# Kernel tuning notes

Measured on AMD Instinct MI355X. Metric: run time of the kernel, lower is better.

The kernel has to match this reference:

```python
import jax, jax.numpy as jnp
import numpy as np

C = 128        # dim_in = dim_out = dim_mid (exp_ratio=1.0)
HEADS = 4      # C // dim_head
DH = 32        # dim_head
WS = 7         # window_size
EPS = 1e-6
SCALE = DH ** -0.5


def bn3d(x, g, b):
    # BatchNorm3d forward (training-mode batch stats), eps=1e-6
    m = jnp.mean(x, axis=(0, 2, 3, 4), keepdims=True)
    v = jnp.mean((x - m) ** 2, axis=(0, 2, 3, 4), keepdims=True)
    xn = (x - m) * jax.lax.rsqrt(v + EPS)
    return xn * g.reshape(1, -1, 1, 1, 1) + b.reshape(1, -1, 1, 1, 1)


def conv1x1(x, w):
    # 1x1x1 conv, no bias: w is (out, in)
    return jnp.einsum('oi,bihwd->bohwd', w, x)


def setup_inputs() -> dict:
    key = jax.random.key(0)
    ks = jax.random.split(key, 6)
    x = jax.random.normal(ks[0], (4, C, 28, 28, 28), jnp.float32)
    g_in = jnp.ones((C,), jnp.float32)
    b_in = jnp.zeros((C,), jnp.float32)
    w_qk = jax.random.normal(ks[1], (2 * C, C), jnp.float32) * (C ** -0.5)
    w_v = jax.random.normal(ks[2], (C, C), jnp.float32) * (C ** -0.5)
    w_cl = jax.random.normal(ks[3], (C, C, 3, 3, 3), jnp.float32) * ((C * 27) ** -0.5)
    g_cl = jnp.ones((C,), jnp.float32)
    b_cl = jnp.zeros((C,), jnp.float32)
    w_proj = jax.random.normal(ks[4], (C, C), jnp.float32) * (C ** -0.5)
    return {"x": x, "g_in": g_in, "b_in": b_in, "w_qk": w_qk, "w_v": w_v,
            "w_cl": w_cl, "g_cl": g_cl, "b_cl": b_cl, "w_proj": w_proj}


def reference(x, g_in, b_in, w_qk, w_v, w_cl, g_cl, b_cl, w_proj):
    B, Cc, H, W, D = x.shape
    shortcut = x
    x = bn3d(x, g_in, b_in)

    # strided window partition: einops '(h1 n1)' => h1 (window) is the OUTER factor
    n1, n2, n3 = H // WS, W // WS, D // WS  # chosen divisible -> zero pad
    xw = x.reshape(B, Cc, WS, n1, WS, n2, WS, n3)
    xw = xw.transpose(0, 3, 5, 7, 1, 2, 4, 6).reshape(B * n1 * n2 * n3, Cc, WS, WS, WS)
    b = xw.shape[0]
    L = WS ** 3

    # qk: 1x1 conv -> split q,k -> (b, heads, L, dh)
    qk = conv1x1(xw, w_qk).reshape(b, 2, HEADS, DH, L)
    q = qk[:, 0].transpose(0, 1, 3, 2)       # b h L d
    k = qk[:, 1]                             # b h d L
    attn = jax.nn.softmax(jnp.einsum('bhld,bhdm->bhlm', q, k) * SCALE, axis=-1)

    # v: 1x1 conv + relu (attn_pre=False)
    v = jax.nn.relu(conv1x1(xw, w_v)).reshape(b, HEADS, DH, L)  # b h d L
    xs = jnp.einsum('bhlm,bhdm->bhld', attn, v)                 # b h L d
    xs = xs.transpose(0, 1, 3, 2).reshape(b, Cc, WS, WS, WS)

    # reverse window partition
    x = xs.reshape(B, n1, n2, n3, Cc, WS, WS, WS)
    x = x.transpose(0, 4, 5, 1, 6, 2, 7, 3).reshape(B, Cc, H, W, D)

    # local 3x3x3 conv + BN + SiLU, residual (has_skip inside iRMB branch)
    y = jax.lax.conv_general_dilated(
        x, w_cl, window_strides=(1, 1, 1),
        padding=[(1, 1), (1, 1), (1, 1)],
        dimension_numbers=('NCDHW', 'OIDHW', 'NCDHW'))
    y = jax.nn.silu(bn3d(y, g_cl, b_cl))
    x = x + y  # SE is Identity (se_ratio=0)

    x = conv1x1(x, w_proj)
    return shortcut + x
```

## Files before the change

### kernel.cpp

```cpp
#include <hip/hip_runtime.h>
#include <hip/hip_bf16.h>

#define C      128
#define SP     21952
#define PT     87808
#define LW     343
#define EPS_   1e-6f
#define SCALE_ 0.17677669529663687f

#define MISC_A   0
#define MISC_B   128
#define MISC_BQK 256
#define MISC_BV  512
#define MISC_SUM 640
#define MISC_SQ  768
#define MISC_A2  896
#define MISC_B2  1024
#define MISC_XS  1152
#define MISC_XQ  1280

typedef __attribute__((ext_vector_type(8))) short bf16x8;
typedef __attribute__((ext_vector_type(4))) float f32x4;

__device__ __forceinline__ float b2f(unsigned short u){
  return __uint_as_float(((unsigned int)u) << 16);
}
__device__ __forceinline__ unsigned short f2b(float f){
  unsigned int u = __float_as_uint(f);
  u += 0x7fffu + ((u >> 16) & 1u);
  return (unsigned short)(u >> 16);
}

__global__ __launch_bounds__(256) void k0_partial(const float* __restrict__ x,
                                                  float* __restrict__ misc){
  int c = blockIdx.x & 127, chunk = blockIdx.x >> 7;
  int bb = chunk >> 1, half = chunk & 1;
  const float4* p = reinterpret_cast<const float4*>(
      x + (size_t)(bb*C + c)*SP + half*10976);
  int t = threadIdx.x;
  float s = 0.f, ss = 0.f;
  for (int i = t; i < 2744; i += 256){
    float4 v = p[i];
    s  += v.x + v.y + v.z + v.w;
    ss += v.x*v.x + v.y*v.y + v.z*v.z + v.w*v.w;
  }
  #pragma unroll
  for (int off = 32; off > 0; off >>= 1){
    s  += __shfl_xor(s,  off);
    ss += __shfl_xor(ss, off);
  }
  __shared__ float red[8];
  int wid = t >> 6, lane = t & 63;
  if (lane == 0){ red[wid] = s; red[4+wid] = ss; }
  __syncthreads();
  if (t == 0){
    atomicAdd(&misc[MISC_XS + c], red[0]+red[1]+red[2]+red[3]);
    atomicAdd(&misc[MISC_XQ + c], red[4]+red[5]+red[6]+red[7]);
  }
}

__global__ void k1_bias(const float* __restrict__ wqk, const float* __restrict__ wvv,
                        const float* __restrict__ gin, const float* __restrict__ bin,
                        float* __restrict__ misc){
  __shared__ float bv[128];
  int t = threadIdx.x;
  {
    float mean = misc[MISC_XS + t] / (float)PT;
    float var  = misc[MISC_XQ + t] / (float)PT - mean*mean;
    float a = rsqrtf(var + EPS_) * gin[t];
    float bb = bin[t] - mean * a;
    bv[t] = bb;
    if (blockIdx.x == 0){ misc[MISC_A + t] = a; misc[MISC_B + t] = bb; }
  }
  __syncthreads();
  int o = blockIdx.x*128 + t;
  float acc = 0.f;
  if (o < 256){
    const float* wr = wqk + (size_t)o*128;
    for (int c = 0; c < 128; ++c) acc += wr[c]*bv[c];
    misc[MISC_BQK + o] = acc;
  } else {
    const float* wr = wvv + (size_t)(o-256)*128;
    for (int c = 0; c < 128; ++c) acc += wr[c]*bv[c];
    misc[MISC_BV + (o-256)] = acc;
  }
}

__global__ void k1w(const float* __restrict__ wqk, const float* __restrict__ wvv,
                    unsigned short* __restrict__ w2){
  int idx = blockIdx.x*256 + threadIdx.x;
  int o = idx >> 7;
  float w = (o < 256) ? wqk[idx] : wvv[idx - 32768];
  unsigned short h = f2b(w);
  w2[idx] = h;
  w2[49152 + idx] = f2b(w - b2f(h));
}

__global__ __launch_bounds__(256) void k2_qkv(const float* __restrict__ x,
        const unsigned short* __restrict__ w2, const float* __restrict__ misc,
        unsigned short* __restrict__ qg, unsigned short* __restrict__ kg,
        unsigned short* __restrict__ vg){
  __shared__ __align__(16) unsigned short xh[8192];
  __shared__ __align__(16) unsigned short xl[8192];
  __shared__ float ascale[128];
  __shared__ unsigned int posTab[64];
  int t = threadIdx.x;
  int P0 = blockIdx.x * 64;
  int b = P0 / SP, sp0 = P0 % SP;
  if (t < 128) ascale[t] = misc[MISC_A + t];
  if (t < 64){
    int sp = sp0 + t;
    int h_ = sp / 784, rem = sp % 784;
    int w_ = rem / 28, d_ = rem % 28;
    int w1 = h_ & 3, s1 = h_ >> 2;
    int w2i = w_ & 3, s2 = w_ >> 2;
    int w3 = d_ & 3, s3 = d_ >> 2;
    int bw = ((b*4 + w1)*4 + w2i)*4 + w3;
    int l  = (s1*7 + s2)*7 + s3;
    posTab[t] = (unsigned int)(bw*43904 + l*32);
  }
  __syncthreads();
  {
    int p = t & 63;
    int ob = t >> 6;
    const float* xb = x + (size_t)b*C*SP + sp0 + p;
    for (int it = 0; it < 4; ++it){
      int c0 = (ob + it*4) * 8;
      unsigned int ph[4], pl[4];
      #pragma unroll
      for (int j = 0; j < 4; ++j){
        float f0 = xb[(size_t)(c0 + 2*j)*SP]     * ascale[c0 + 2*j];
        float f1 = xb[(size_t)(c0 + 2*j + 1)*SP] * ascale[c0 + 2*j + 1];
        unsigned short h0 = f2b(f0), h1 = f2b(f1);
        unsigned short l0 = f2b(f0 - b2f(h0)), l1 = f2b(f1 - b2f(h1));
        ph[j] = (unsigned int)h0 | ((unsigned int)h1 << 16);
        pl[j] = (unsigned int)l0 | ((unsigned int)l1 << 16);
      }
      int byte = (p*256 + c0*2) ^ ((p & 7) << 4);
      *reinterpret_cast<uint4*>((char*)xh + byte) = make_uint4(ph[0],ph[1],ph[2],ph[3]);
      *reinterpret_cast<uint4*>((char*)xl + byte) = make_uint4(pl[0],pl[1],pl[2],pl[3]);
    }
  }
  __syncthreads();
  int wid = t >> 6, lane = t & 63;
  int g = lane >> 4, ln = lane & 15;
  int wstart = wid * 96;
  f32x4 acc[6][4];
  #pragma unroll
  for (int nt = 0; nt < 6; ++nt){
    float bv = misc[256 + wstart + nt*16 + ln];
    #pragma unroll
    for (int mt = 0; mt < 4; ++mt) acc[nt][mt] = (f32x4){bv,bv,bv,bv};
  }
  #pragma unroll 1
  for (int kk = 0; kk < 4; ++kk){
    bf16x8 ah[4], al[4];
    #pragma unroll
    for (int mt = 0; mt < 4; ++mt){
      int row = mt*16 + ln;
      int byte = (row*256 + kk*64 + g*16) ^ ((ln & 7) << 4);
      ah[mt] = *reinterpret_cast<const bf16x8*>((const char*)xh + byte);
      al[mt] = *reinterpret_cast<const bf16x8*>((const char*)xl + byte);
    }
    #pragma unroll
    for (int nt = 0; nt < 6; ++nt){
      int o = wstart + nt*16 + ln;
      const unsigned short* wp = w2 + (size_t)o*128 + kk*32 + g*8;
      bf16x8 whf = *reinterpret_cast<const bf16x8*>(wp);
      bf16x8 wlf = *reinterpret_cast<const bf16x8*>(wp + 49152);
      #pragma unroll
      for (int mt = 0; mt < 4; ++mt){
        acc[nt][mt] = __builtin_amdgcn_mfma_f32_16x16x32_bf16(ah[mt], whf, acc[nt][mt], 0, 0, 0);
        acc[nt][mt] = __builtin_amdgcn_mfma_f32_16x16x32_bf16(al[mt], whf, acc[nt][mt], 0, 0, 0);
        acc[nt][mt] = __builtin_amdgcn_mfma_f32_16x16x32_bf16(ah[mt], wlf, acc[nt][mt], 0, 0, 0);
      }
    }
  }
  unsigned int ptab[16];
  #pragma unroll
  for (int mt = 0; mt < 4; ++mt)
    #pragma unroll
    for (int r = 0; r < 4; ++r)
      ptab[mt*4+r] = posTab[mt*16 + g*4 + r];
  #pragma unroll
  for (int nt = 0; nt < 6; ++nt){
    int o = wstart + nt*16 + ln;
    bool isv = (o >= 256);
    int oo = o & 127;
    unsigned short* dst = ((o < 128) ? qg : (o < 256 ? kg : vg)) + (oo >> 5)*10976 + (oo & 31);
    #pragma unroll
    for (int mt = 0; mt < 4; ++mt){
      #pragma unroll
      for (int r = 0; r < 4; ++r){
        float v = acc[nt][mt][r];
        if (isv) v = fmaxf(v, 0.f);
        dst[ptab[mt*4+r]] = f2b(v);
      }
    }
  }
}

__global__ __launch_bounds__(256) void k3_attn(const unsigned short* __restrict__ qg,
        const unsigned short* __restrict__ kg, const unsigned short* __restrict__ vg,
        unsigned short* __restrict__ xatt){
  __shared__ __align__(16) unsigned short klds[352*32];
  __shared__ __align__(16) unsigned short vper[32*360];
  __shared__ __align__(16) unsigned short pbuf[4][640];
  int bh = blockIdx.x;
  int bw = bh >> 2, h = bh & 3;
  int t = threadIdx.x;
  int wid = t >> 6, lane = t & 63;
  int g = lane >> 4, ln = lane & 15;
  const unsigned short* kbase = kg + (size_t)bh*LW*32;
  const unsigned short* vbase = vg + (size_t)bh*LW*32;
  const unsigned short* qbase = qg + (size_t)bh*LW*32;
  {
    const uint4* src = reinterpret_cast<const uint4*>(kbase);
    uint4* dst = reinterpret_cast<uint4*>(klds);
    for (int i = t; i < 1372; i += 256) dst[i] = src[i];
    for (int i = t; i < 288; i += 256) klds[10976 + i] = 0;
  }
  for (int idx = t; idx < 10976; idx += 256){
    int m = idx >> 5, d = idx & 31;
    int km = m & 31;
    int pk = ((km & 15) << 1) | (km >> 4);
    vper[d*360 + ((m >> 5) << 5) + pk] = vbase[idx];
  }
  for (int i = t; i < 288; i += 256){
    int m = 343 + (i >> 5), d = i & 31;
    int km = m & 31;
    int pk = ((km & 15) << 1) | (km >> 4);
    vper[d*360 + 320 + pk] = 0;
  }
  __syncthreads();
  int w1 = (bw>>4)&3, w2 = (bw>>2)&3, w3 = bw&3, b = bw>>6;
  unsigned short* pb = pbuf[wid];
  const f32x4 zero4 = {0.f, 0.f, 0.f, 0.f};
  for (int rt = wid; rt < 22; rt += 4){
    int row0 = rt << 4;
    bf16x8 qf = *reinterpret_cast<const bf16x8*>(qbase + (size_t)(row0 + ln)*32 + g*8);
    f32x4 s[22];
    #pragma unroll
    for (int nt = 0; nt < 22; ++nt){
      bf16x8 kf = *reinterpret_cast<const bf16x8*>(&klds[(nt*16 + ln)*32 + g*8]);
      s[nt] = __builtin_amdgcn_mfma_f32_16x16x32_bf16(qf, kf, zero4, 0, 0, 0);
    }
    float mxs[4];
    #pragma unroll
    for (int q = 0; q < 4; ++q){
      float m0 = -1e30f;
      #pragma unroll
      for (int nt = 0; nt < 21; ++nt) m0 = fmaxf(m0, s[nt][q]);
      if (ln < 7) m0 = fmaxf(m0, s[21][q]);
      #pragma unroll
      for (int off = 8; off > 0; off >>= 1) m0 = fmaxf(m0, __shfl_xor(m0, off));
      mxs[q] = m0 * SCALE_;
    }
    f32x4 o0 = zero4, o1 = zero4;
    float sums[4] = {0.f, 0.f, 0.f, 0.f};
    #pragma unroll
    for (int c = 0; c < 11; ++c){
      #pragma unroll
      for (int q = 0; q < 4; ++q){
        float e0 = __expf(fmaf(s[2*c][q],   SCALE_, -mxs[q]));
        float e1 = (c*32 + 16 + ln < 343)
                 ? __expf(fmaf(s[2*c+1][q], SCALE_, -mxs[q])) : 0.f;
        sums[q] += e0 + e1;
        unsigned int pkd;
        asm volatile("v_cvt_pk_bf16_f32 %0, %1, %2" : "=v"(pkd) : "v"(e0), "v"(e1));
        *reinterpret_cast<unsigned int*>(&pb[(g*4+q)*40 + (ln<<1)]) = pkd;
      }
      asm volatile("s_waitcnt lgkmcnt(0)" ::: "memory");
      __builtin_amdgcn_sched_barrier(0);
      bf16x8 pa  = *reinterpret_cast<const bf16x8*>(&pb[ln*40 + g*8]);
      bf16x8 vb0 = *reinterpret_cast<const bf16x8*>(&vper[ln*360       + (c<<5) + g*8]);
      bf16x8 vb1 = *reinterpret_cast<const bf16x8*>(&vper[(16+ln)*360  + (c<<5) + g*8]);
      o0 = __builtin_amdgcn_mfma_f32_16x16x32_bf16(pa, vb0, o0, 0, 0, 0);
      o1 = __builtin_amdgcn_mfma_f32_16x16x32_bf16(pa, vb1, o1, 0, 0, 0);
    }
    float iss[4];
    #pragma unroll
    for (int q = 0; q < 4; ++q){
      float sq = sums[q];
      #pragma unroll
      for (int off = 8; off > 0; off >>= 1) sq += __shfl_xor(sq, off);
      iss[q] = 1.f / sq;
    }
    #pragma unroll
    for (int q = 0; q < 4; ++q){
      int l = row0 + g*4 + q;
      if (l < 343){
        int ss1 = l/49, ss2 = (l/7)%7, ss3 = l%7;
        int sp = (ss1*4+w1)*784 + (ss2*4+w2)*28 + (ss3*4+w3);
        size_t gaddr = ((size_t)b*SP + sp)*128 + h*32;
        xatt[gaddr + ln]      = f2b(o0[q]*iss[q]);
        xatt[gaddr + 16 + ln] = f2b(o1[q]*iss[q]);
      }
    }
  }
}

__global__ void k_wprep(const float* __restrict__ wcl, unsigned short* __restrict__ wbf){
  int f = blockIdx.x*256 + threadIdx.x;
  int j  = f & 7;
  int oc = (f >> 3) & 127;
  int kgr= (f >> 10) & 7;
  int sl = f >> 13;
  int h  = sl / 27, tap = sl % 27;
  int ic = h*64 + kgr*8 + j;
  wbf[f] = f2b(wcl[((size_t)oc*128 + ic)*27 + tap]);
}

__global__ void k6w(const float* __restrict__ wproj, unsigned short* __restrict__ w6){
  int idx = blockIdx.x*256 + threadIdx.x;
  float w = wproj[idx];
  unsigned short h = f2b(w);
  w6[idx] = h;
  w6[16384 + idx] = f2b(w - b2f(h));
}

__global__ __launch_bounds__(256, 3) void k4_mfma(const unsigned short* __restrict__ xag,
        const unsigned short* __restrict__ wbf, unsigned short* __restrict__ yg){
  __shared__ __align__(16) unsigned char smem[32768];
  unsigned short* halo = (unsigned short*)smem;
  float* redf = (float*)smem;
  int t = threadIdx.x, wid = t >> 6, lane = t & 63;
  int g = lane >> 4, ln = lane & 15;
  int ks = wid & 1, ohalf = wid >> 1;
  int hp = (ln>>2)*6 + (ln&3);
  unsigned int vbase = (unsigned int)((ks*4096 + g*1024 + ohalf*512 + ln*8) * 2);
  bf16x8 bA[4], bB[4];
  f32x4 acc[4][4];

  #define BISSUE(dst_, sl_) do { \
    unsigned int vo_ = vbase + (unsigned int)(sl_) * 16384u; \
    asm volatile("global_load_dwordx4 %0, %1, %2"            : "=v"(dst_[0]) : "v"(vo_), "s"(wbf)); \
    asm volatile("global_load_dwordx4 %0, %1, %2 offset:256" : "=v"(dst_[1]) : "v"(vo_), "s"(wbf)); \
    asm volatile("global_load_dwordx4 %0, %1, %2 offset:512" : "=v"(dst_[2]) : "v"(vo_), "s"(wbf)); \
    asm volatile("global_load_dwordx4 %0, %1, %2 offset:768" : "=v"(dst_[3]) : "v"(vo_), "s"(wbf)); \
  } while(0)

  #define ALOAD(dst_, tap_) do { \
    int dz_ = (tap_)/9, r9_ = (tap_)%9, dy_ = r9_/3, dx_ = r9_%3; \
    int off_ = dz_*36 + dy_*6 + dx_; \
    _Pragma("unroll") \
    for (int mt_ = 0; mt_ < 4; ++mt_) \
      dst_[mt_] = *reinterpret_cast<const bf16x8*>( \
          &halo[((ks*4 + g)*216 + mt_*36 + hp + off_)*8]); \
  } while(0)

  #define COMPUTER(a_, b_) do { \
    _Pragma("unroll") \
    for (int nt_ = 0; nt_ < 4; ++nt_) \
      _Pragma("unroll") \
      for (int mt_ = 0; mt_ < 4; ++mt_) \
        acc[nt_][mt_] = __builtin_amdgcn_mfma_f32_16x16x32_bf16( \
            a_[mt_], b_[nt_], acc[nt_][mt_], 0, 0, 0); \
  } while(0)

  #define BWAIT4() do { \
    asm volatile("s_waitcnt vmcnt(4)"); \
    __builtin_amdgcn_sched_barrier(0); \
  } while(0)
  #define BWAIT0() do { \
    asm volatile("s_waitcnt vmcnt(0)"); \
    __builtin_amdgcn_sched_barrier(0); \
  } while(0)

  for (int s = blockIdx.x; s < 1372; s += 768){
    int b = s / 343, srem = s % 343;
    int z0 = (srem/49)*4, y0 = ((srem/7)%7)*4, x0 = (srem%7)*4;
    #pragma unroll
    for (int nt = 0; nt < 4; ++nt)
      #pragma unroll
      for (int mt = 0; mt < 4; ++mt)
        acc[nt][mt] = (f32x4){0.f, 0.f, 0.f, 0.f};
    for (int h = 0; h < 2; ++h){
      __syncthreads();
      for (int ci = t; ci < 1728; ci += 256){
        int kgr = ci / 216, pos = ci % 216;
        int uz = pos / 36, r36 = pos % 36, uy = r36 / 6, ux = r36 % 6;
        int zz = z0 - 1 + uz, yy = y0 - 1 + uy, xx = x0 - 1 + ux;
        uint4 v = make_uint4(0u,0u,0u,0u);
        if (zz >= 0 && zz < 28 && yy >= 0 && yy < 28 && xx >= 0 && xx < 28)
          v = *reinterpret_cast<const uint4*>(
                &xag[(((size_t)b*SP) + zz*784 + yy*28 + xx)*128 + h*64 + kgr*8]);
        *reinterpret_cast<uint4*>(&halo[(size_t)ci*8]) = v;
      }
      __syncthreads();
      int sw = h*27;
      bf16x8 af0[4], af1[4];
      BISSUE(bA, sw);
      #pragma unroll 1
      for (int tp = 0; tp < 26; tp += 2){
        BISSUE(bB, sw+tp+1);
        ALOAD(af0, tp);
        BWAIT4();
        COMPUTER(af0, bA);
        BISSUE(bA, sw+tp+2);
        ALOAD(af1, tp+1);
        BWAIT4();
        COMPUTER(af1, bB);
      }
      ALOAD(af0, 26);
      BWAIT0();
      COMPUTER(af0, bA);
    }
    __syncthreads();
    if (ks == 1){
      #pragma unroll
      for (int nt = 0; nt < 4; ++nt)
        #pragma unroll
        for (int mt = 0; mt < 4; ++mt)
          *reinterpret_cast<f32x4*>(
              &redf[(((ohalf*16 + nt*4 + mt)*64) + lane)*4]) = acc[nt][mt];
    }
    __syncthreads();
    if (ks == 0){
      #pragma unroll
      for (int nt = 0; nt < 4; ++nt){
        int oc = ohalf*64 + nt*16 + ln;
        #pragma unroll
        for (int mt = 0; mt < 4; ++mt){
          f32x4 other = *reinterpret_cast<const f32x4*>(
              &redf[(((ohalf*16 + nt*4 + mt)*64) + lane)*4]);
          f32x4 tot = acc[nt][mt] + other;
          #pragma unroll
          for (int r = 0; r < 4; ++r){
            int pos = (z0 + mt)*784 + (y0 + g)*28 + (x0 + r);
            yg[((size_t)b*SP + pos)*128 + oc] = f2b(tot[r]);
          }
        }
      }
    }
  }
  #undef BISSUE
  #undef ALOAD
  #undef COMPUTER
  #undef BWAIT4
  #undef BWAIT0
}

__global__ __launch_bounds__(256) void k5_ystats(const unsigned short* __restrict__ yg,
                                                 float* __restrict__ misc){
  int t = threadIdx.x;
  int c8 = t & 15;
  int pr = t >> 4;
  float s[8] = {0,0,0,0,0,0,0,0}, q[8] = {0,0,0,0,0,0,0,0};
  size_t base = (size_t)blockIdx.x * 256;
  for (int i = 0; i < 16; ++i){
    size_t pos = base + i*16 + pr;
    uint4 v = *reinterpret_cast<const uint4*>(yg + pos*128 + c8*8);
    #pragma unroll
    for (int j = 0; j < 4; ++j){
      unsigned int u = (&v.x)[j];
      float f0 = __uint_as_float(u << 16);
      float f1 = __uint_as_float(u & 0xffff0000u);
      s[2*j]   += f0; q[2*j]   += f0*f0;
      s[2*j+1] += f1; q[2*j+1] += f1*f1;
    }
  }
  #pragma unroll
  for (int j = 0; j < 8; ++j){
    s[j] += __shfl_xor(s[j], 16); q[j] += __shfl_xor(q[j], 16);
    s[j] += __shfl_xor(s[j], 32); q[j] += __shfl_xor(q[j], 32);
  }
  __shared__ float rs[128], rq[128];
  if (t < 128){ rs[t] = 0.f; rq[t] = 0.f; }
  __syncthreads();
  if ((t & 48) == 0){
    #pragma unroll
    for (int j = 0; j < 8; ++j){
      atomicAdd(&rs[c8*8+j], s[j]);
      atomicAdd(&rq[c8*8+j], q[j]);
    }
  }
  __syncthreads();
  if (t < 128){
    atomicAdd(&misc[MISC_SUM + t], rs[t]);
    atomicAdd(&misc[MISC_SQ  + t], rq[t]);
  }
}

__global__ void k5b_finstats(const float* __restrict__ gcl, const float* __restrict__ bcl,
                             float* __restrict__ misc){
  int c = threadIdx.x;
  float mean = misc[MISC_SUM+c] / (float)PT;
  float var  = misc[MISC_SQ +c] / (float)PT - mean*mean;
  float a = gcl[c] * rsqrtf(var + EPS_);
  misc[MISC_A2+c] = a;
  misc[MISC_B2+c] = bcl[c] - mean*a;
}

__global__ __launch_bounds__(256) void k6_final(const unsigned short* __restrict__ xag,
        const unsigned short* __restrict__ yg, const unsigned short* __restrict__ w6,
        const float* __restrict__ xin, const float* __restrict__ misc,
        float* __restrict__ out){
  __shared__ __align__(16) unsigned short xh[8192];
  __shared__ __align__(16) unsigned short xl[8192];
  __shared__ float a2s[128], b2s[128];
  int t = threadIdx.x;
  int P0 = blockIdx.x * 64;
  int b = P0 / SP, sp0 = P0 % SP;
  if (t < 128){ a2s[t] = misc[MISC_A2+t]; b2s[t] = misc[MISC_B2+t]; }
  __syncthreads();
  for (int idx = t; idx < 1024; idx += 256){
    int p = idx >> 4, c0 = (idx & 15) * 8;
    size_t gb = (size_t)(P0 + p)*128 + c0;
    uint4 yv4 = *reinterpret_cast<const uint4*>(yg + gb);
    uint4 xa4 = *reinterpret_cast<const uint4*>(xag + gb);
    unsigned int ph[4], pl[4];
    #pragma unroll
    for (int j = 0; j < 4; ++j){
      unsigned int uy = (&yv4.x)[j], ux = (&xa4.x)[j];
      int c = c0 + 2*j;
      float y0 = __uint_as_float(uy << 16)          * a2s[c]   + b2s[c];
      float y1 = __uint_as_float(uy & 0xffff0000u)  * a2s[c+1] + b2s[c+1];
      float v0 = __uint_as_float(ux << 16)         + y0 / (1.f + __expf(-y0));
      float v1 = __uint_as_float(ux & 0xffff0000u) + y1 / (1.f + __expf(-y1));
      unsigned short h0 = f2b(v0), h1 = f2b(v1);
      unsigned short l0 = f2b(v0 - b2f(h0)), l1 = f2b(v1 - b2f(h1));
      ph[j] = (unsigned int)h0 | ((unsigned int)h1 << 16);
      pl[j] = (unsigned int)l0 | ((unsigned int)l1 << 16);
    }
    int byte = (p*256 + c0*2) ^ ((p & 7) << 4);
    *reinterpret_cast<uint4*>((char*)xh + byte) = make_uint4(ph[0],ph[1],ph[2],ph[3]);
    *reinterpret_cast<uint4*>((char*)xl + byte) = make_uint4(pl[0],pl[1],pl[2],pl[3]);
  }
  __syncthreads();
  int wid = t >> 6, lane = t & 63;
  int g = lane >> 4, ln = lane & 15;
  f32x4 acc[2][4] = {};
  #pragma unroll 1
  for (int kk = 0; kk < 4; ++kk){
    bf16x8 bh[4], bl[4];
    #pragma unroll
    for (int pt = 0; pt < 4; ++pt){
      int row = pt*16 + ln;
      int byte = (row*256 + kk*64 + g*16) ^ ((ln & 7) << 4);
      bh[pt] = *reinterpret_cast<const bf16x8*>((const char*)xh + byte);
      bl[pt] = *reinterpret_cast<const bf16x8*>((const char*)xl + byte);
    }
    #pragma unroll
    for (int ot = 0; ot < 2; ++ot){
      int o = wid*32 + ot*16 + ln;
      const unsigned short* wp = w6 + (size_t)o*128 + kk*32 + g*8;
      bf16x8 wh = *reinterpret_cast<const bf16x8*>(wp);
      bf16x8 wl = *reinterpret_cast<const bf16x8*>(wp + 16384);
      #pragma unroll
      for (int pt = 0; pt < 4; ++pt){
        acc[ot][pt] = __builtin_amdgcn_mfma_f32_16x16x32_bf16(wh, bh[pt], acc[ot][pt], 0, 0, 0);
        acc[ot][pt] = __builtin_amdgcn_mfma_f32_16x16x32_bf16(wl, bh[pt], acc[ot][pt], 0, 0, 0);
        acc[ot][pt] = __builtin_amdgcn_mfma_f32_16x16x32_bf16(wh, bl[pt], acc[ot][pt], 0, 0, 0);
      }
    }
  }
  #pragma unroll
  for (int ot = 0; ot < 2; ++ot){
    #pragma unroll
    for (int r = 0; r < 4; ++r){
      int o = wid*32 + ot*16 + g*4 + r;
      size_t gbase = ((size_t)b*128 + o)*SP + sp0;
      #pragma unroll
      for (int pt = 0; pt < 4; ++pt){
        size_t gaddr = gbase + pt*16 + ln;
        out[gaddr] = xin[gaddr] + acc[ot][pt][r];
      }
    }
  }
}

extern "C" void kernel_launch(void* const* d_in, const int* in_sizes, int n_in,
                              void* d_out, int out_size, void* d_ws, size_t ws_size,
                              hipStream_t stream){
  const float* x      = (const float*)d_in[0];
  const float* g_in   = (const float*)d_in[1];
  const float* b_in   = (const float*)d_in[2];
  const float* w_qk   = (const float*)d_in[3];
  const float* w_v    = (const float*)d_in[4];
  const float* w_cl   = (const float*)d_in[5];
  const float* g_cl   = (const float*)d_in[6];
  const float* b_cl   = (const float*)d_in[7];
  const float* w_proj = (const float*)d_in[8];
  float* out = (float*)d_out;

  char* ws = (char*)d_ws;
  unsigned short* qg  = (unsigned short*)ws;
  unsigned short* kgp = qg  + 11239424;
  unsigned short* vg  = kgp + 11239424;
  unsigned short* xag = vg  + 11239424;
  unsigned short* yg  = xag + 11239424;
  float* misc = (float*)(ws + (size_t)5*22478848);
  unsigned short* wbf = qg;
  unsigned short* w6  = qg + 524288;
  unsigned short* w2  = yg;

  hipMemsetAsync(misc + MISC_SUM, 0, 768*sizeof(float), stream);
  k0_partial  <<<1024, 256, 0, stream>>>(x, misc);
  k1_bias     <<<3, 128, 0, stream>>>(w_qk, w_v, g_in, b_in, misc);
  k1w         <<<192, 256, 0, stream>>>(w_qk, w_v, w2);
  k2_qkv      <<<1372, 256, 0, stream>>>(x, w2, misc, qg, kgp, vg);
  k3_attn     <<<1024, 256, 0, stream>>>(qg, kgp, vg, xag);
  k_wprep     <<<1728, 256, 0, stream>>>(w_cl, wbf);
  k6w         <<<64, 256, 0, stream>>>(w_proj, w6);
  k4_mfma     <<<768, 256, 0, stream>>>(xag, wbf, yg);
  k5_ystats   <<<343, 256, 0, stream>>>(yg, misc);
  k5b_finstats<<<1, 128, 0, stream>>>(g_cl, b_cl, misc);
  k6_final    <<<1372, 256, 0, stream>>>(xag, yg, w6, x, misc, out);
}
```

Baseline: 363.3 us.

## Repartition conv MFMA warps over spatial rows and vectorize V transpose loads

The 3x3x3 conv kernel now splits work across warps by spatial z-halves covering all 128 output channels, rather than by output-channel halves covering all spatial rows. Each warp loads twice as many weight fragments per tap from global memory (8 instead of 4) and half as many halo activation fragments from LDS. Weight prefetch depth doubles accordingly. The attention kernel's V transpose into LDS now uses 16-byte global loads scattered into eight shorts, instead of one scalar load per element. The trade is more global weight traffic and registers per warp in exchange for fewer LDS reads, which may affect occupancy under launch_bounds(256,3).

Result: slower. 387.2 us (+6.6%).

```diff
diff --git a/kernel.cpp b/kernel.cpp
--- a/kernel.cpp
+++ b/kernel.cpp
@@ -220,11 +220,24 @@
     for (int i = t; i < 1372; i += 256) dst[i] = src[i];
     for (int i = t; i < 288; i += 256) klds[10976 + i] = 0;
   }
-  for (int idx = t; idx < 10976; idx += 256){
-    int m = idx >> 5, d = idx & 31;
-    int km = m & 31;
-    int pk = ((km & 15) << 1) | (km >> 4);
-    vper[d*360 + ((m >> 5) << 5) + pk] = vbase[idx];
+  {
+    const uint4* v4 = reinterpret_cast<const uint4*>(vbase);
+    for (int idx = t; idx < 1372; idx += 256){
+      int m = idx >> 2, d0 = (idx & 3) * 8;
+      uint4 v = v4[idx];
+      int km = m & 31;
+      int pk = ((km & 15) << 1) | (km >> 4);
+      int col = ((m >> 5) << 5) + pk;
+      unsigned short* dp = &vper[(size_t)d0*360 + col];
+      dp[0*360] = (unsigned short)(v.x & 0xffffu);
+      dp[1*360] = (unsigned short)(v.x >> 16);
+      dp[2*360] = (unsigned short)(v.y & 0xffffu);
+      dp[3*360] = (unsigned short)(v.y >> 16);
+      dp[4*360] = (unsigned short)(v.z & 0xffffu);
+      dp[5*360] = (unsigned short)(v.z >> 16);
+      dp[6*360] = (unsigned short)(v.w & 0xffffu);
+      dp[7*360] = (unsigned short)(v.w >> 16);
+    }
   }
   for (int i = t; i < 288; i += 256){
     int m = 343 + (i >> 5), d = i & 31;
@@ -326,40 +339,44 @@
   float* redf = (float*)smem;
   int t = threadIdx.x, wid = t >> 6, lane = t & 63;
   int g = lane >> 4, ln = lane & 15;
-  int ks = wid & 1, ohalf = wid >> 1;
+  int ks = wid & 1, mh = wid >> 1;
   int hp = (ln>>2)*6 + (ln&3);
-  unsigned int vbase = (unsigned int)((ks*4096 + g*1024 + ohalf*512 + ln*8) * 2);
-  bf16x8 bA[4], bB[4];
-  f32x4 acc[4][4];
+  unsigned int vbase = (unsigned int)(((ks*4 + g)*1024 + ln*8) * 2);
+  bf16x8 bA[8], bB[8];
+  f32x4 acc[8][2];
 
   #define BISSUE(dst_, sl_) do { \
     unsigned int vo_ = vbase + (unsigned int)(sl_) * 16384u; \
-    asm volatile("global_load_dwordx4 %0, %1, %2"            : "=v"(dst_[0]) : "v"(vo_), "s"(wbf)); \
-    asm volatile("global_load_dwordx4 %0, %1, %2 offset:256" : "=v"(dst_[1]) : "v"(vo_), "s"(wbf)); \
-    asm volatile("global_load_dwordx4 %0, %1, %2 offset:512" : "=v"(dst_[2]) : "v"(vo_), "s"(wbf)); \
-    asm volatile("global_load_dwordx4 %0, %1, %2 offset:768" : "=v"(dst_[3]) : "v"(vo_), "s"(wbf)); \
+    asm volatile("global_load_dwordx4 %0, %1, %2"             : "=v"(dst_[0]) : "v"(vo_), "s"(wbf)); \
+    asm volatile("global_load_dwordx4 %0, %1, %2 offset:256"  : "=v"(dst_[1]) : "v"(vo_), "s"(wbf)); \
+    asm volatile("global_load_dwordx4 %0, %1, %2 offset:512"  : "=v"(dst_[2]) : "v"(vo_), "s"(wbf)); \
+    asm volatile("global_load_dwordx4 %0, %1, %2 offset:768"  : "=v"(dst_[3]) : "v"(vo_), "s"(wbf)); \
+    asm volatile("global_load_dwordx4 %0, %1, %2 offset:1024" : "=v"(dst_[4]) : "v"(vo_), "s"(wbf)); \
+    asm volatile("global_load_dwordx4 %0, %1, %2 offset:1280" : "=v"(dst_[5]) : "v"(vo_), "s"(wbf)); \
+    asm volatile("global_load_dwordx4 %0, %1, %2 offset:1536" : "=v"(dst_[6]) : "v"(vo_), "s"(wbf)); \
+    asm volatile("global_load_dwordx4 %0, %1, %2 offset:1792" : "=v"(dst_[7]) : "v"(vo_), "s"(wbf)); \
   } while(0)
 
   #define ALOAD(dst_, tap_) do { \
     int dz_ = (tap_)/9, r9_ = (tap_)%9, dy_ = r9_/3, dx_ = r9_%3; \
     int off_ = dz_*36 + dy_*6 + dx_; \
     _Pragma("unroll") \
-    for (int mt_ = 0; mt_ < 4; ++mt_) \
-      dst_[mt_] = *reinterpret_cast<const bf16x8*>( \
-          &halo[((ks*4 + g)*216 + mt_*36 + hp + off_)*8]); \
+    for (int mti_ = 0; mti_ < 2; ++mti_) \
+      dst_[mti_] = *reinterpret_cast<const bf16x8*>( \
+          &halo[((ks*4 + g)*216 + (mh*2 + mti_)*36 + hp + off_)*8]); \
   } while(0)
 
   #define COMPUTER(a_, b_) do { \
     _Pragma("unroll") \
-    for (int nt_ = 0; nt_ < 4; ++nt_) \
+    for (int nt_ = 0; nt_ < 8; ++nt_) \
       _Pragma("unroll") \
-      for (int mt_ = 0; mt_ < 4; ++mt_) \
-        acc[nt_][mt_] = __builtin_amdgcn_mfma_f32_16x16x32_bf16( \
-            a_[mt_], b_[nt_], acc[nt_][mt_], 0, 0, 0); \
+      for (int mti_ = 0; mti_ < 2; ++mti_) \
+        acc[nt_][mti_] = __builtin_amdgcn_mfma_f32_16x16x32_bf16( \
+            a_[mti_], b_[nt_], acc[nt_][mti_], 0, 0, 0); \
   } while(0)
 
-  #define BWAIT4() do { \
-    asm volatile("s_waitcnt vmcnt(4)"); \
+  #define BWAIT8() do { \
+    asm volatile("s_waitcnt vmcnt(8)"); \
     __builtin_amdgcn_sched_barrier(0); \
   } while(0)
   #define BWAIT0() do { \
@@ -371,10 +388,10 @@
     int b = s / 343, srem = s % 343;
     int z0 = (srem/49)*4, y0 = ((srem/7)%7)*4, x0 = (srem%7)*4;
     #pragma unroll
-    for (int nt = 0; nt < 4; ++nt)
-      #pragma unroll
-      for (int mt = 0; mt < 4; ++mt)
-        acc[nt][mt] = (f32x4){0.f, 0.f, 0.f, 0.f};
+    for (int nt = 0; nt < 8; ++nt)
+      #pragma unroll
+      for (int mti = 0; mti < 2; ++mti)
+        acc[nt][mti] = (f32x4){0.f, 0.f, 0.f, 0.f};
     for (int h = 0; h < 2; ++h){
       __syncthreads();
       for (int ci = t; ci < 1728; ci += 256){
@@ -389,17 +406,17 @@
       }
       __syncthreads();
       int sw = h*27;
-      bf16x8 af0[4], af1[4];
+      bf16x8 af0[2], af1[2];
       BISSUE(bA, sw);
       #pragma unroll 1
       for (int tp = 0; tp < 26; tp += 2){
         BISSUE(bB, sw+tp+1);
         ALOAD(af0, tp);
-        BWAIT4();
+        BWAIT8();
         COMPUTER(af0, bA);
         BISSUE(bA, sw+tp+2);
         ALOAD(af1, tp+1);
-        BWAIT4();
+        BWAIT8();
         COMPUTER(af1, bB);
       }
       ALOAD(af0, 26);
@@ -409,25 +426,25 @@
     __syncthreads();
     if (ks == 1){
       #pragma unroll
-      for (int nt = 0; nt < 4; ++nt)
+      for (int nt = 0; nt < 8; ++nt)
         #pragma unroll
-        for (int mt = 0; mt < 4; ++mt)
+        for (int mti = 0; mti < 2; ++mti)
           *reinterpret_cast<f32x4*>(
-              &redf[(((ohalf*16 + nt*4 + mt)*64) + lane)*4]) = acc[nt][mt];
+              &redf[(((mh*16 + nt*2 + mti)*64) + lane)*4]) = acc[nt][mti];
     }
     __syncthreads();
     if (ks == 0){
       #pragma unroll
-      for (int nt = 0; nt < 4; ++nt){
-        int oc = ohalf*64 + nt*16 + ln;
+      for (int nt = 0; nt < 8; ++nt){
+        int oc = nt*16 + ln;
         #pragma unroll
-        for (int mt = 0; mt < 4; ++mt){
+        for (int mti = 0; mti < 2; ++mti){
           f32x4 other = *reinterpret_cast<const f32x4*>(
-              &redf[(((ohalf*16 + nt*4 + mt)*64) + lane)*4]);
-          f32x4 tot = acc[nt][mt] + other;
+              &redf[(((mh*16 + nt*2 + mti)*64) + lane)*4]);
+          f32x4 tot = acc[nt][mti] + other;
           #pragma unroll
           for (int r = 0; r < 4; ++r){
-            int pos = (z0 + mt)*784 + (y0 + g)*28 + (x0 + r);
+            int pos = (z0 + mh*2 + mti)*784 + (y0 + g)*28 + (x0 + r);
             yg[((size_t)b*SP + pos)*128 + oc] = f2b(tot[r]);
           }
         }
@@ -437,7 +454,7 @@
   #undef BISSUE
   #undef ALOAD
   #undef COMPUTER
-  #undef BWAIT4
+  #undef BWAIT8
   #undef BWAIT0
 }
 
```
